# Performance work log

Measured on AMD Instinct MI355X. Metric: run time of the kernel, lower is better.

Reference implementation:

```python
import jax, jax.numpy as jnp
import numpy as np

B, L, H, D, VOC, C, P = 16, 256, 6, 768, 32000, 20, 1
d = D // H
MAXF = 20
BN_EPS = 1e-5


def setup_inputs() -> dict:
    key = jax.random.key(0)
    ks = jax.random.split(key, 8)
    doc_tids = jax.random.randint(ks[0], (B, L), 0, VOC)
    TFs = jax.random.uniform(ks[1], (B, L), dtype=jnp.float32) * 20.0 + 1.0
    DFs = jax.random.uniform(ks[2], (B, L), dtype=jnp.float32) * 1000.0 + 1.0
    emb = jax.random.normal(ks[3], (VOC, D), dtype=jnp.float32) * 0.02
    fcW = jax.random.normal(ks[4], (C + P, D), dtype=jnp.float32) * 0.02
    fcb = jnp.zeros((C + P,), dtype=jnp.float32)
    weiW = jax.random.normal(ks[5], (2, H), dtype=jnp.float32) * 0.1
    weib = jnp.zeros((2,), dtype=jnp.float32)
    return dict(doc_tids=doc_tids, TFs=TFs, DFs=DFs, emb=emb,
                fcW=fcW, fcb=fcb, weiW=weiW, weib=weib)


def _bn(x):
    # BatchNorm over channel axis 1 (H), batch stats over all other axes (train mode, affine=False)
    m = x.mean(axis=(0, 2, 3), keepdims=True)
    v = x.var(axis=(0, 2, 3), keepdims=True)
    return (x - m) * jax.lax.rsqrt(v + BN_EPS)


def _leaky9(x):
    return jnp.where(x >= 0, x, 9.0 * x)


def reference(doc_tids, TFs, DFs, emb, fcW, fcb, weiW, weib):
    # --- EmbbedingTFIDF (eval mode, dropout off): tf-idf weighted embedding lookup ---
    tf = jnp.minimum(TFs, float(MAXF))
    idf = jnp.log1p(1.0 / DFs)
    x = emb[doc_tids] * (tf * idf)[:, :, None]          # (B, L, D)
    valid = doc_tids != 0
    # model flips pad_mask with logical_not, then co_weights[pad_mask] = 0
    invalid = ~(valid[:, :, None] & valid[:, None, :])  # (B, L, L) True -> zero out
    mask = invalid[:, None, :, :]                       # broadcast over heads

    def split_heads(h):
        return h.reshape(B, L, H, d).transpose(0, 2, 1, 3)  # (B, H, L, d)

    Q = split_heads(x)
    K = Q
    V = Q

    # --- nearAttention (layers=1) ---
    Vn = _bn(V)
    # DistMatrix: pairwise Euclidean distance dist[b,h,i,j] = ||K_i - Q_j||
    Ksq = jnp.sum(K * K, axis=-1)[..., :, None]
    Qsq = jnp.sum(Q * Q, axis=-1)[..., None, :]
    cross = jnp.einsum('bhid,bhjd->bhij', K, Q)
    co = jnp.sqrt(jnp.maximum(Ksq + Qsq - 2.0 * cross, 1e-12))  # (B, H, L, L)
    # BatchNorm1d(H) over flattened (B, H, L*L) == per-H stats over (0,2,3)
    co = _leaky9(_bn(co))
    co = jnp.where(mask, 0.0, co)
    co = jax.nn.softmax(co, axis=-1)
    co = jnp.where(jnp.isnan(co), 0.0, co)
    V_out = jnp.einsum('bhij,bhjd->bhid', co, Vn)
    Q_out = _bn(jnp.einsum('bhij,bhjd->bhid', co, Q))
    K_out = _bn(jnp.einsum('bhij,bhjd->bhid', co, K))

    # --- head ---
    Vc = V_out.transpose(0, 2, 1, 3).reshape(B, L, D)       # catHiddens
    V_lgts = jax.nn.softmax(Vc @ fcW.T + fcb, axis=-1)      # (B, L, C+P)
    cw = jnp.swapaxes(co, -1, -2).reshape(B, L * L, H)      # transpose then contiguous reshape
    cw = jax.nn.softmax(cw @ weiW.T + weib, axis=-1)        # (B, L*L, 2)
    cw = cw.reshape(B, L, L, 2).sum(axis=-2, keepdims=True)[:, :, :, 0]  # (B, L, 1)
    cw = jax.nn.softmax(cw, axis=-1)                        # softmax over singleton -> ones (faithful)
    logits = (cw * V_lgts).sum(axis=1)[:, :C]               # (B, C)
    logits = jax.nn.softmax(logits, axis=-1)
    return logits
```

## Files before the change

kernel.cpp:

```cpp
#include <hip/hip_runtime.h>
#include <hip/hip_bf16.h>
#include <math.h>

#define OFF_XH   0UL
#define OFF_XT   1572864UL
#define OFF_VC   3145728UL
#define OFF_SQ   4718592UL
#define OFF_THS  4743168UL
#define OFF_PART 4767744UL
#define OFF_STAT 4780032UL
#define OFF_ACC  4780056UL
#define OFF_CTR  4780392UL
#define OFF_FCWB 4780396UL

typedef __attribute__((ext_vector_type(8))) __bf16 bf16x8;
typedef __attribute__((ext_vector_type(4))) float f32x4;
typedef __attribute__((ext_vector_type(8))) unsigned short u16x8;

__global__ __launch_bounds__(512) void k12_fused(const int* __restrict__ tids,
    const float* __restrict__ TF, const float* __restrict__ DF,
    const float* __restrict__ emb, unsigned short* __restrict__ xh,
    unsigned short* __restrict__ xT, float* __restrict__ sq,
    float* __restrict__ ths, float* __restrict__ part) {
  int jh = blockIdx.x, bh = blockIdx.y;
  int b = bh / 6, h = bh % 6;
  int tid = threadIdx.x;
  __shared__ unsigned short tile[32768];
  if (tid < 2) part[((size_t)bh * 2 + jh) * 2 + tid] = 0.0f;
  int sub = tid & 7, row0 = tid >> 3;
  int c16 = sub * 16;
#pragma unroll
  for (int p = 0; p < 4; ++p) {
    int r = p * 64 + row0;
    int tok = b * 256 + r;
    int tv = tids[tok];
    float wgt = fminf(TF[tok], 20.0f) * log1pf(1.0f / DF[tok]);
    const float* er = emb + (size_t)tv * 768 + h * 128 + c16;
    float4 e0 = *(const float4*)er;
    float4 e1 = *(const float4*)(er + 4);
    float4 e2 = *(const float4*)(er + 8);
    float4 e3 = *(const float4*)(er + 12);
    float f[16] = {e0.x, e0.y, e0.z, e0.w, e1.x, e1.y, e1.z, e1.w,
                   e2.x, e2.y, e2.z, e2.w, e3.x, e3.y, e3.z, e3.w};
    u16x8 pk0, pk1;
    float s1 = 0.0f, s2 = 0.0f;
#pragma unroll
    for (int e = 0; e < 8; ++e) {
      __hip_bfloat16 hb = __float2bfloat16(f[e] * wgt);
      float g = __bfloat162float(hb);
      s1 += g; s2 += g * g;
      pk0[e] = __bfloat16_as_ushort(hb);
    }
#pragma unroll
    for (int e = 0; e < 8; ++e) {
      __hip_bfloat16 hb = __float2bfloat16(f[8 + e] * wgt);
      float g = __bfloat162float(hb);
      s1 += g; s2 += g * g;
      pk1[e] = __bfloat16_as_ushort(hb);
    }
    int rx = r & 7;
    *(u16x8*)&tile[r * 128 + (((sub * 2    ) ^ rx) * 8)] = pk0;
    *(u16x8*)&tile[r * 128 + (((sub * 2 + 1) ^ rx) * 8)] = pk1;
    if (jh == 0) {
      unsigned short* xo = xh + ((size_t)bh * 256 + r) * 128 + c16;
      *(u16x8*)xo = pk0;
      *(u16x8*)(xo + 8) = pk1;
    }
    s1 += __shfl_down(s1, 4); s1 += __shfl_down(s1, 2); s1 += __shfl_down(s1, 1);
    s2 += __shfl_down(s2, 4); s2 += __shfl_down(s2, 2); s2 += __shfl_down(s2, 1);
    if (sub == 0) {
      sq[(size_t)bh * 256 + r] = s2;
      if (jh == 0) ths[(size_t)bh * 256 + r] = s1;
    }
  }
  __syncthreads();
  if (jh == 1) {
    int ch = tid & 127, q = tid >> 7;
    int cc = ch >> 3, cs = ch & 7;
    unsigned int* xo = (unsigned int*)xT + ((size_t)bh * 128 + ch) * 128 + q * 32;
#pragma unroll
    for (int g = 0; g < 8; ++g) {
      unsigned int tmp[4];
#pragma unroll
      for (int k = 0; k < 4; ++k) {
        int t0 = q * 64 + (g * 4 + k) * 2;
        unsigned int lo = tile[ t0      * 128 + ((cc ^ ( t0      & 7)) * 8) + cs];
        unsigned int hi = tile[(t0 + 1) * 128 + ((cc ^ ((t0 + 1) & 7)) * 8) + cs];
        tmp[k] = lo | (hi << 16);
      }
      uint4 vv; vv.x = tmp[0]; vv.y = tmp[1]; vv.z = tmp[2]; vv.w = tmp[3];
      *(uint4*)(xo + g * 4) = vv;
    }
  }
  int w = tid >> 6, lane = tid & 63, quad = lane >> 4, l16 = lane & 15;
  const float* sqh = sq + (size_t)bh * 256;
  int it0 = w * 2;
  bf16x8 a2[2][4];
  float si2[2][4];
#pragma unroll
  for (int ith = 0; ith < 2; ++ith) {
    int ar = (it0 + ith) * 16 + l16, arx = ar & 7;
#pragma unroll
    for (int k0 = 0; k0 < 4; ++k0)
      a2[ith][k0] = *(const bf16x8*)&tile[ar * 128 + (((k0 * 4 + quad) ^ arx) * 8)];
#pragma unroll
    for (int r = 0; r < 4; ++r)
      si2[ith][r] = sqh[(it0 + ith) * 16 + quad * 4 + r];
  }
  float ls1 = 0.0f, ls2 = 0.0f;
#pragma unroll
  for (int jt = 0; jt < 8; ++jt) {
    int jr = jh * 128 + jt * 16 + l16, jrx = jr & 7;
    bf16x8 bfr[4];
#pragma unroll
    for (int k0 = 0; k0 < 4; ++k0)
      bfr[k0] = *(const bf16x8*)&tile[jr * 128 + (((k0 * 4 + quad) ^ jrx) * 8)];
    f32x4 acc0 = {0.0f, 0.0f, 0.0f, 0.0f}, acc1 = {0.0f, 0.0f, 0.0f, 0.0f};
#pragma unroll
    for (int k0 = 0; k0 < 4; ++k0) {
      acc0 = __builtin_amdgcn_mfma_f32_16x16x32_bf16(a2[0][k0], bfr[k0], acc0, 0, 0, 0);
      acc1 = __builtin_amdgcn_mfma_f32_16x16x32_bf16(a2[1][k0], bfr[k0], acc1, 0, 0, 0);
    }
    float sj = sqh[jr];
#pragma unroll
    for (int r = 0; r < 4; ++r) {
      float cv0 = sqrtf(fmaxf(si2[0][r] + sj - 2.0f * acc0[r], 1e-12f));
      float cv1 = sqrtf(fmaxf(si2[1][r] + sj - 2.0f * acc1[r], 1e-12f));
      ls1 += cv0 + cv1;
      ls2 += cv0 * cv0 + cv1 * cv1;
    }
  }
#pragma unroll
  for (int off = 32; off >= 1; off >>= 1) {
    ls1 += __shfl_down(ls1, off);
    ls2 += __shfl_down(ls2, off);
  }
  if (lane == 0) {
    atomicAdd(&part[((size_t)bh * 2 + jh) * 2 + 0], ls1);
    atomicAdd(&part[((size_t)bh * 2 + jh) * 2 + 1], ls2);
  }
}

__global__ __launch_bounds__(384) void k3_stats(const float* __restrict__ ths,
    const float* __restrict__ sq, const float* __restrict__ part,
    const float* __restrict__ fcW, float* __restrict__ stats,
    float* __restrict__ acc, unsigned int* __restrict__ ctr,
    unsigned short* __restrict__ fcWb) {
  int h = threadIdx.x >> 6, lane = threadIdx.x & 63;
  float s1 = 0.0f, s2 = 0.0f;
  for (int m = 0; m < 64; ++m) {
    int f = m * 64 + lane;
    int bb = f >> 8, l = f & 255;
    size_t idx = ((size_t)(bb * 6 + h)) * 256 + l;
    s1 += ths[idx]; s2 += sq[idx];
  }
#pragma unroll
  for (int off = 32; off >= 1; off >>= 1) {
    s1 += __shfl_down(s1, off);
    s2 += __shfl_down(s2, off);
  }
  if (lane == 0) {
    float cnt = 524288.0f;
    float mean = s1 / cnt;
    float var = s2 / cnt - mean * mean;
    stats[h] = mean;
    stats[6 + h] = rsqrtf(var + 1e-5f);
  }
  float c1 = 0.0f, c2 = 0.0f;
  if (lane < 32) {
    int bb = lane >> 1, jh = lane & 1;
    size_t pidx = (((size_t)(bb * 6 + h)) * 2 + jh) * 2;
    c1 = part[pidx]; c2 = part[pidx + 1];
  }
#pragma unroll
  for (int off = 16; off >= 1; off >>= 1) {
    c1 += __shfl_down(c1, off);
    c2 += __shfl_down(c2, off);
  }
  if (lane == 0) {
    float cnt = 1048576.0f;
    float mean = c1 / cnt;
    float var = c2 / cnt - mean * mean;
    stats[12 + h] = mean;
    stats[18 + h] = rsqrtf(var + 1e-5f);
  }
  if (threadIdx.x < 336) acc[threadIdx.x] = 0.0f;
  if (threadIdx.x == 336) *ctr = 0u;
  for (int idx = threadIdx.x; idx < 21 * 768; idx += 384)
    fcWb[idx] = __bfloat16_as_ushort(__float2bfloat16(fcW[idx]));
}

__global__ __launch_bounds__(256, 4) void k45_fused(const unsigned short* __restrict__ xh,
    const unsigned short* __restrict__ xT, const int* __restrict__ tids,
    const float* __restrict__ sq, const float* __restrict__ stats,
    unsigned short* __restrict__ vc16) {
  int p = blockIdx.x, bh = blockIdx.y;
  int b = bh / 6, h = bh % 6;
  int tid = threadIdx.x, w = tid >> 6, lane = tid & 63;
  int quad = lane >> 4, l16 = lane & 15;
  int I = p * 16;
  __shared__ float svld[256];
  __shared__ float ssq[256];
  __shared__ unsigned short cot[16][264];
  __shared__ float smax[16][4];
  __shared__ float ssum[16][4];
  svld[tid] = (tids[b * 256 + tid] != 0) ? 1.0f : 0.0f;
  ssq[tid] = sq[(size_t)bh * 256 + tid];
  const __bf16* xb = (const __bf16*)xh + (size_t)bh * 256 * 128;
  bf16x8 a[4];
#pragma unroll
  for (int k0 = 0; k0 < 4; ++k0)
    a[k0] = *(const bf16x8*)(xb + (size_t)(I + l16) * 128 + k0 * 32 + quad * 8);
  __syncthreads();
  float m = stats[12 + h], rsc = stats[18 + h];
  float rv[4], si[4];
#pragma unroll
  for (int r = 0; r < 4; ++r) {
    rv[r] = svld[I + quad * 4 + r];
    si[r] = ssq[I + quad * 4 + r];
  }
  float y[4][4];
#pragma unroll
  for (int tl = 0; tl < 4; ++tl) {
    int t = w * 4 + tl;
    f32x4 acc = {0.0f, 0.0f, 0.0f, 0.0f};
#pragma unroll
    for (int k0 = 0; k0 < 4; ++k0) {
      bf16x8 bfr = *(const bf16x8*)(xb + (size_t)(t * 16 + l16) * 128 + k0 * 32 + quad * 8);
      acc = __builtin_amdgcn_mfma_f32_16x16x32_bf16(a[k0], bfr, acc, 0, 0, 0);
    }
    float sj = ssq[t * 16 + l16];
    float cvld = svld[t * 16 + l16];
#pragma unroll
    for (int r = 0; r < 4; ++r) {
      float cv = sqrtf(fmaxf(si[r] + sj - 2.0f * acc[r], 1e-12f));
      float yv = (cv - m) * rsc;
      yv = yv >= 0.0f ? yv : 9.0f * yv;
      y[tl][r] = yv * rv[r] * cvld;
    }
  }
#pragma unroll
  for (int r = 0; r < 4; ++r) {
    float mx = fmaxf(fmaxf(y[0][r], y[1][r]), fmaxf(y[2][r], y[3][r]));
#pragma unroll
    for (int off = 1; off <= 8; off <<= 1) mx = fmaxf(mx, __shfl_xor(mx, off));
    if (l16 == 0) smax[quad * 4 + r][w] = mx;
  }
  __syncthreads();
  float gmx[4];
#pragma unroll
  for (int r = 0; r < 4; ++r) {
    int row = quad * 4 + r;
    gmx[r] = fmaxf(fmaxf(smax[row][0], smax[row][1]), fmaxf(smax[row][2], smax[row][3]));
    float s = 0.0f;
#pragma unroll
    for (int tl = 0; tl < 4; ++tl) { y[tl][r] = expf(y[tl][r] - gmx[r]); s += y[tl][r]; }
#pragma unroll
    for (int off = 1; off <= 8; off <<= 1) s += __shfl_xor(s, off);
    if (l16 == 0) ssum[row][w] = s;
  }
  __syncthreads();
#pragma unroll
  for (int r = 0; r < 4; ++r) {
    int row = quad * 4 + r;
    float gs = ssum[row][0] + ssum[row][1] + ssum[row][2] + ssum[row][3];
    float inv = 1.0f / gs;
#pragma unroll
    for (int tl = 0; tl < 4; ++tl)
      cot[row][w * 64 + tl * 16 + l16] =
          __bfloat16_as_ushort(__float2bfloat16(y[tl][r] * inv));
  }
  __syncthreads();
  bf16x8 a2[8];
#pragma unroll
  for (int k0 = 0; k0 < 8; ++k0)
    a2[k0] = *(const bf16x8*)&cot[l16][k0 * 32 + quad * 8];
  const __bf16* xbT = (const __bf16*)xT + (size_t)bh * 128 * 256;
  float mv = stats[h], rvs = stats[6 + h];
  float rm = rvs * mv;
  size_t vbase = ((size_t)(b * 256 + I + quad * 4)) * 768 + h * 128;
#pragma unroll
  for (int jl = 0; jl < 2; ++jl) {
    int ch = (w * 2 + jl) * 16 + l16;
    const __bf16* brow = xbT + (size_t)ch * 256;
    f32x4 vacc = {0.0f, 0.0f, 0.0f, 0.0f};
#pragma unroll
    for (int k0 = 0; k0 < 8; ++k0) {
      bf16x8 bfr = *(const bf16x8*)(brow + k0 * 32 + quad * 8);
      vacc = __builtin_amdgcn_mfma_f32_16x16x32_bf16(a2[k0], bfr, vacc, 0, 0, 0);
    }
#pragma unroll
    for (int r = 0; r < 4; ++r) {
      float ov = rvs * vacc[r] - rm;
      vc16[vbase + (size_t)r * 768 + ch] = __bfloat16_as_ushort(__float2bfloat16(ov));
    }
  }
}

__global__ __launch_bounds__(256) void k5b6_lgts(const unsigned short* __restrict__ vc16,
    const unsigned short* __restrict__ fcWb, const float* __restrict__ fcb,
    float* __restrict__ acc, unsigned int* __restrict__ ctr, float* __restrict__ out) {
  int b = blockIdx.x >> 2, qa = blockIdx.x & 3;
  int tid = threadIdx.x, w = tid >> 6, lane = tid & 63;
  int quad = lane >> 4, l16 = lane & 15;
  int tok0 = b * 256 + qa * 64 + w * 16;
  int c1c = (l16 < 5) ? (16 + l16) : 20;
  const __bf16* vb = (const __bf16*)vc16;
  const __bf16* w0 = (const __bf16*)fcWb + (size_t)l16 * 768;
  const __bf16* w1 = (const __bf16*)fcWb + (size_t)c1c * 768;
  f32x4 ac0 = {0.0f, 0.0f, 0.0f, 0.0f}, ac1 = {0.0f, 0.0f, 0.0f, 0.0f};
#pragma unroll
  for (int k0 = 0; k0 < 24; ++k0) {
    int ko = k0 * 32 + quad * 8;
    bf16x8 af = *(const bf16x8*)(vb + (size_t)(tok0 + l16) * 768 + ko);
    bf16x8 b0 = *(const bf16x8*)(w0 + ko);
    bf16x8 b1 = *(const bf16x8*)(w1 + ko);
    ac0 = __builtin_amdgcn_mfma_f32_16x16x32_bf16(af, b0, ac0, 0, 0, 0);
    ac1 = __builtin_amdgcn_mfma_f32_16x16x32_bf16(af, b1, ac1, 0, 0, 0);
  }
  float bias0 = fcb[l16];
  float bias1 = (l16 < 5) ? fcb[16 + l16] : 0.0f;
  float p0s = 0.0f, p1s = 0.0f;
#pragma unroll
  for (int r = 0; r < 4; ++r) {
    float lg0 = ac0[r] + bias0;
    float lg1 = (l16 < 5) ? (ac1[r] + bias1) : -1e30f;
    float mx = fmaxf(lg0, lg1);
#pragma unroll
    for (int off = 1; off <= 8; off <<= 1) mx = fmaxf(mx, __shfl_xor(mx, off));
    float e0 = expf(lg0 - mx), e1 = expf(lg1 - mx);
    float s = e0 + e1;
#pragma unroll
    for (int off = 1; off <= 8; off <<= 1) s += __shfl_xor(s, off);
    float inv = 1.0f / s;
    p0s += e0 * inv;
    p1s += e1 * inv;
  }
  p0s += __shfl_xor(p0s, 16); p0s += __shfl_xor(p0s, 32);
  p1s += __shfl_xor(p1s, 16); p1s += __shfl_xor(p1s, 32);
  __shared__ float sacc[4][21];
  __shared__ unsigned int sdone;
  if (quad == 0) sacc[w][l16] = p0s;
  if (quad == 1 && l16 < 5) sacc[w][16 + l16] = p1s;
  __syncthreads();
  if (tid < 21) {
    float s = sacc[0][tid] + sacc[1][tid] + sacc[2][tid] + sacc[3][tid];
    atomicAdd(&acc[b * 21 + tid], s);
  }
  __syncthreads();
  if (tid == 0) {
    __threadfence();
    sdone = atomicAdd(ctr, 1u);
  }
  __syncthreads();
  if (sdone == 63u && tid < 16) {
    float v[20];
    float mx = -1e30f;
#pragma unroll
    for (int c = 0; c < 20; ++c) {
      v[c] = atomicAdd(&acc[tid * 21 + c], 0.0f);
      mx = fmaxf(mx, v[c]);
    }
    float s = 0.0f;
#pragma unroll
    for (int c = 0; c < 20; ++c) { v[c] = expf(v[c] - mx); s += v[c]; }
    float inv = 1.0f / s;
#pragma unroll
    for (int c = 0; c < 20; ++c) out[tid * 20 + c] = v[c] * inv;
  }
}

extern "C" void kernel_launch(void* const* d_in, const int* in_sizes, int n_in,
                              void* d_out, int out_size, void* d_ws, size_t ws_size,
                              hipStream_t stream) {
  const int*   tids = (const int*)d_in[0];
  const float* TF   = (const float*)d_in[1];
  const float* DF   = (const float*)d_in[2];
  const float* emb  = (const float*)d_in[3];
  const float* fcW  = (const float*)d_in[4];
  const float* fcb  = (const float*)d_in[5];
  float* out = (float*)d_out;
  float* ws  = (float*)d_ws;
  unsigned short* xh   = (unsigned short*)(ws + OFF_XH);
  unsigned short* xT   = (unsigned short*)(ws + OFF_XT);
  unsigned short* vc   = (unsigned short*)(ws + OFF_VC);
  unsigned short* fcWb = (unsigned short*)(ws + OFF_FCWB);
  float* sq    = ws + OFF_SQ;
  float* ths   = ws + OFF_THS;
  float* part  = ws + OFF_PART;
  float* stats = ws + OFF_STAT;
  float* acc   = ws + OFF_ACC;
  unsigned int* ctr = (unsigned int*)(ws + OFF_CTR);

  k12_fused<<<dim3(2, 96), 512, 0, stream>>>(tids, TF, DF, emb, xh, xT, sq, ths, part);
  k3_stats<<<1, 384, 0, stream>>>(ths, sq, part, fcW, stats, acc, ctr, fcWb);
  k45_fused<<<dim3(16, 96), 256, 0, stream>>>(xh, xT, tids, sq, stats, vc);
  k5b6_lgts<<<64, 256, 0, stream>>>(vc, fcWb, fcb, acc, ctr, out);
}
```

Baseline: 207.4 us.

## Eliminate single-block stats kernel by folding reductions into neighbouring kernels

```diff
diff --git a/kernel.cpp b/kernel.cpp
--- a/kernel.cpp
+++ b/kernel.cpp
@@ -21,14 +21,26 @@
     const float* __restrict__ TF, const float* __restrict__ DF,
     const float* __restrict__ emb, unsigned short* __restrict__ xh,
     unsigned short* __restrict__ xT, float* __restrict__ sq,
-    float* __restrict__ ths, float* __restrict__ part) {
+    float* __restrict__ part, const float* __restrict__ fcW,
+    unsigned short* __restrict__ fcWb, float* __restrict__ acc,
+    unsigned int* __restrict__ ctr) {
   int jh = blockIdx.x, bh = blockIdx.y;
   int b = bh / 6, h = bh % 6;
   int tid = threadIdx.x;
   __shared__ unsigned short tile[32768];
-  if (tid < 2) part[((size_t)bh * 2 + jh) * 2 + tid] = 0.0f;
+  __shared__ float swd1[8], swd2[8], swv1[8], swv2[8];
+  if (jh == 1) {
+    if (tid < 168) {
+      int idx = bh * 168 + tid;
+      fcWb[idx] = __bfloat16_as_ushort(__float2bfloat16(fcW[idx]));
+    }
+  } else if (bh == 0) {
+    if (tid < 336) acc[tid] = 0.0f;
+    if (tid == 336) *ctr = 0u;
+  }
   int sub = tid & 7, row0 = tid >> 3;
   int c16 = sub * 16;
+  float ts1 = 0.0f, ts2 = 0.0f;
 #pragma unroll
   for (int p = 0; p < 4; ++p) {
     int r = p * 64 + row0;
@@ -58,6 +70,7 @@
       s1 += g; s2 += g * g;
       pk1[e] = __bfloat16_as_ushort(hb);
     }
+    ts1 += s1; ts2 += s2;
     int rx = r & 7;
     *(u16x8*)&tile[r * 128 + (((sub * 2    ) ^ rx) * 8)] = pk0;
     *(u16x8*)&tile[r * 128 + (((sub * 2 + 1) ^ rx) * 8)] = pk1;
@@ -66,12 +79,9 @@
       *(u16x8*)xo = pk0;
       *(u16x8*)(xo + 8) = pk1;
     }
-    s1 += __shfl_down(s1, 4); s1 += __shfl_down(s1, 2); s1 += __shfl_down(s1, 1);
     s2 += __shfl_down(s2, 4); s2 += __shfl_down(s2, 2); s2 += __shfl_down(s2, 1);
-    if (sub == 0) {
+    if (sub == 0)
       sq[(size_t)bh * 256 + r] = s2;
-      if (jh == 0) ths[(size_t)bh * 256 + r] = s1;
-    }
   }
   __syncthreads();
   if (jh == 1) {
@@ -134,67 +144,29 @@
   for (int off = 32; off >= 1; off >>= 1) {
     ls1 += __shfl_down(ls1, off);
     ls2 += __shfl_down(ls2, off);
-  }
-  if (lane == 0) {
-    atomicAdd(&part[((size_t)bh * 2 + jh) * 2 + 0], ls1);
-    atomicAdd(&part[((size_t)bh * 2 + jh) * 2 + 1], ls2);
-  }
-}
-
-__global__ __launch_bounds__(384) void k3_stats(const float* __restrict__ ths,
-    const float* __restrict__ sq, const float* __restrict__ part,
-    const float* __restrict__ fcW, float* __restrict__ stats,
-    float* __restrict__ acc, unsigned int* __restrict__ ctr,
-    unsigned short* __restrict__ fcWb) {
-  int h = threadIdx.x >> 6, lane = threadIdx.x & 63;
-  float s1 = 0.0f, s2 = 0.0f;
-  for (int m = 0; m < 64; ++m) {
-    int f = m * 64 + lane;
-    int bb = f >> 8, l = f & 255;
-    size_t idx = ((size_t)(bb * 6 + h)) * 256 + l;
-    s1 += ths[idx]; s2 += sq[idx];
-  }
-#pragma unroll
-  for (int off = 32; off >= 1; off >>= 1) {
-    s1 += __shfl_down(s1, off);
-    s2 += __shfl_down(s2, off);
-  }
-  if (lane == 0) {
-    float cnt = 524288.0f;
-    float mean = s1 / cnt;
-    float var = s2 / cnt - mean * mean;
-    stats[h] = mean;
-    stats[6 + h] = rsqrtf(var + 1e-5f);
-  }
-  float c1 = 0.0f, c2 = 0.0f;
-  if (lane < 32) {
-    int bb = lane >> 1, jh = lane & 1;
-    size_t pidx = (((size_t)(bb * 6 + h)) * 2 + jh) * 2;
-    c1 = part[pidx]; c2 = part[pidx + 1];
-  }
-#pragma unroll
-  for (int off = 16; off >= 1; off >>= 1) {
-    c1 += __shfl_down(c1, off);
-    c2 += __shfl_down(c2, off);
-  }
-  if (lane == 0) {
-    float cnt = 1048576.0f;
-    float mean = c1 / cnt;
-    float var = c2 / cnt - mean * mean;
-    stats[12 + h] = mean;
-    stats[18 + h] = rsqrtf(var + 1e-5f);
-  }
-  if (threadIdx.x < 336) acc[threadIdx.x] = 0.0f;
-  if (threadIdx.x == 336) *ctr = 0u;
-  for (int idx = threadIdx.x; idx < 21 * 768; idx += 384)
-    fcWb[idx] = __bfloat16_as_ushort(__float2bfloat16(fcW[idx]));
+    ts1 += __shfl_down(ts1, off);
+    ts2 += __shfl_down(ts2, off);
+  }
+  if (lane == 0) { swd1[w] = ls1; swd2[w] = ls2; swv1[w] = ts1; swv2[w] = ts2; }
+  __syncthreads();
+  if (tid == 0) {
+    float d1 = 0.0f, d2 = 0.0f, v1 = 0.0f, v2 = 0.0f;
+#pragma unroll
+    for (int i = 0; i < 8; ++i) { d1 += swd1[i]; d2 += swd2[i]; v1 += swv1[i]; v2 += swv2[i]; }
+    part[192 + (bh * 2 + jh) * 2 + 0] = d1;
+    part[192 + (bh * 2 + jh) * 2 + 1] = d2;
+    if (jh == 0) { part[bh * 2] = v1; part[bh * 2 + 1] = v2; }
+  }
 }
 
 __global__ __launch_bounds__(256, 4) void k45_fused(const unsigned short* __restrict__ xh,
     const unsigned short* __restrict__ xT, const int* __restrict__ tids,
-    const float* __restrict__ sq, const float* __restrict__ stats,
+    const float* __restrict__ sq, const float* __restrict__ part,
     unsigned short* __restrict__ vc16) {
-  int p = blockIdx.x, bh = blockIdx.y;
+  int bid = blockIdx.x;
+  int xcd = bid & 7, idx = bid >> 3;
+  int bh = xcd * 12 + idx % 12;
+  int p = idx / 12;
   int b = bh / 6, h = bh % 6;
   int tid = threadIdx.x, w = tid >> 6, lane = tid & 63;
   int quad = lane >> 4, l16 = lane & 15;
@@ -204,15 +176,49 @@
   __shared__ unsigned short cot[16][264];
   __shared__ float smax[16][4];
   __shared__ float ssum[16][4];
+  __shared__ float sstat[4];
   svld[tid] = (tids[b * 256 + tid] != 0) ? 1.0f : 0.0f;
   ssq[tid] = sq[(size_t)bh * 256 + tid];
+  if (w == 0) {
+    float c1 = 0.0f, c2 = 0.0f;
+    if (lane < 32) {
+      int bb = lane >> 1, jj = lane & 1;
+      c1 = part[192 + ((bb * 6 + h) * 2 + jj) * 2 + 0];
+      c2 = part[192 + ((bb * 6 + h) * 2 + jj) * 2 + 1];
+    }
+#pragma unroll
+    for (int off = 16; off >= 1; off >>= 1) {
+      c1 += __shfl_down(c1, off);
+      c2 += __shfl_down(c2, off);
+    }
+    float v1 = 0.0f, v2 = 0.0f;
+    if (lane < 16) {
+      v1 = part[(lane * 6 + h) * 2 + 0];
+      v2 = part[(lane * 6 + h) * 2 + 1];
+    }
+#pragma unroll
+    for (int off = 8; off >= 1; off >>= 1) {
+      v1 += __shfl_down(v1, off);
+      v2 += __shfl_down(v2, off);
+    }
+    if (lane == 0) {
+      float mean = c1 / 1048576.0f;
+      float var = c2 / 1048576.0f - mean * mean;
+      sstat[0] = mean;
+      sstat[1] = rsqrtf(var + 1e-5f);
+      float mv = v1 / 524288.0f;
+      float vv = v2 / 524288.0f - mv * mv;
+      sstat[2] = mv;
+      sstat[3] = rsqrtf(vv + 1e-5f);
+    }
+  }
   const __bf16* xb = (const __bf16*)xh + (size_t)bh * 256 * 128;
   bf16x8 a[4];
 #pragma unroll
   for (int k0 = 0; k0 < 4; ++k0)
     a[k0] = *(const bf16x8*)(xb + (size_t)(I + l16) * 128 + k0 * 32 + quad * 8);
   __syncthreads();
-  float m = stats[12 + h], rsc = stats[18 + h];
+  float m = sstat[0], rsc = sstat[1];
   float rv[4], si[4];
 #pragma unroll
   for (int r = 0; r < 4; ++r) {
@@ -276,7 +282,7 @@
   for (int k0 = 0; k0 < 8; ++k0)
     a2[k0] = *(const bf16x8*)&cot[l16][k0 * 32 + quad * 8];
   const __bf16* xbT = (const __bf16*)xT + (size_t)bh * 128 * 256;
-  float mv = stats[h], rvs = stats[6 + h];
+  float mv = sstat[2], rvs = sstat[3];
   float rm = rvs * mv;
   size_t vbase = ((size_t)(b * 256 + I + quad * 4)) * 768 + h * 128;
 #pragma unroll
@@ -386,14 +392,12 @@
   unsigned short* vc   = (unsigned short*)(ws + OFF_VC);
   unsigned short* fcWb = (unsigned short*)(ws + OFF_FCWB);
   float* sq    = ws + OFF_SQ;
-  float* ths   = ws + OFF_THS;
   float* part  = ws + OFF_PART;
-  float* stats = ws + OFF_STAT;
   float* acc   = ws + OFF_ACC;
   unsigned int* ctr = (unsigned int*)(ws + OFF_CTR);
 
-  k12_fused<<<dim3(2, 96), 512, 0, stream>>>(tids, TF, DF, emb, xh, xT, sq, ths, part);
-  k3_stats<<<1, 384, 0, stream>>>(ths, sq, part, fcW, stats, acc, ctr, fcWb);
-  k45_fused<<<dim3(16, 96), 256, 0, stream>>>(xh, xT, tids, sq, stats, vc);
+  k12_fused<<<dim3(2, 96), 512, 0, stream>>>(tids, TF, DF, emb, xh, xT, sq, part,
+                                             fcW, fcWb, acc, ctr);
+  k45_fused<<<1536, 256, 0, stream>>>(xh, xT, tids, sq, part, vc);
   k5b6_lgts<<<64, 256, 0, stream>>>(vc, fcWb, fcb, acc, ctr, out);
 }
```

New measurement: 193.6 us. 6.7% less time.
